# Performance work log

Hardware: AMD Instinct MI355X
Metric: run time of the kernel (lower is better)

## Reference

```python
import jax, jax.numpy as jnp
import numpy as np

B, S, DIM, HEADS, DHEAD = 1, 1992, 2048, 16, 128
NKI_SEQ_ALIGN = 128
EPS = 1e-6


def setup_inputs() -> dict:
    key = jax.random.key(0)
    ks = jax.random.split(key, 8)
    hidden_states = jax.random.normal(ks[0], (B, S, DIM), dtype=jnp.float32)
    # realistic rotary tables, full head_dim with interleaved pair angles
    pos = jnp.arange(S, dtype=jnp.float32)
    inv_freq = 1.0 / (10000.0 ** (jnp.arange(0, DHEAD, 2, dtype=jnp.float32) / DHEAD))
    ang = pos[:, None] * inv_freq[None, :]                      # [S, DHEAD/2]
    full = jnp.stack([ang, ang], axis=-1).reshape(S, DHEAD)     # interleave
    freqs_cos = jnp.cos(full)[None, :, None, :]                 # [1,S,1,DHEAD]
    freqs_sin = jnp.sin(full)[None, :, None, :]
    sc = 0.02
    wq = jax.random.normal(ks[1], (DIM, DIM), dtype=jnp.float32) * sc
    wk = jax.random.normal(ks[2], (DIM, DIM), dtype=jnp.float32) * sc
    wv = jax.random.normal(ks[3], (DIM, DIM), dtype=jnp.float32) * sc
    wo = jax.random.normal(ks[4], (DIM, DIM), dtype=jnp.float32) * sc
    bq = jax.random.normal(ks[5], (DIM,), dtype=jnp.float32) * sc
    bk = jax.random.normal(ks[6], (DIM,), dtype=jnp.float32) * sc
    bv = jax.random.normal(ks[7], (DIM,), dtype=jnp.float32) * sc
    bo = jnp.zeros((DIM,), dtype=jnp.float32)
    norm_q_w = jnp.ones((DIM,), dtype=jnp.float32)
    norm_k_w = jnp.ones((DIM,), dtype=jnp.float32)
    return dict(hidden_states=hidden_states, freqs_cos=freqs_cos, freqs_sin=freqs_sin,
                wq=wq, bq=bq, wk=wk, bk=bk, wv=wv, bv=bv,
                norm_q_w=norm_q_w, norm_k_w=norm_k_w, wo=wo, bo=bo)


def _rms_norm(x, weight, eps=EPS):
    xf = x.astype(jnp.float32)
    var = jnp.mean(xf * xf, axis=-1, keepdims=True)
    return (weight * (xf * jax.lax.rsqrt(var + eps))).astype(x.dtype)


def _apply_rope(x, freqs_cos, freqs_sin):
    # x: [B,H,S,D]; freqs: [1,S,1,D]
    cos = jnp.transpose(freqs_cos[..., 0::2], (0, 2, 1, 3))  # [1,1,S,D/2]
    sin = jnp.transpose(freqs_sin[..., 1::2], (0, 2, 1, 3))
    x1, x2 = x[..., 0::2], x[..., 1::2]
    o1 = x1 * cos - x2 * sin
    o2 = x1 * sin + x2 * cos
    return jnp.stack([o1, o2], axis=-1).reshape(x.shape)


def _attention_padded(q, k, v):
    # Faithful to nki_flash_attention: zero-pad seq to multiple of 128,
    # no masking of padded keys (they contribute logit 0), trim query pad.
    B_, H_, S_, D_ = q.shape
    pad = (-S_) % NKI_SEQ_ALIGN
    if pad:
        pc = [(0, 0), (0, 0), (0, pad), (0, 0)]
        q = jnp.pad(q, pc); k = jnp.pad(k, pc); v = jnp.pad(v, pc)
    scale = 1.0 / np.sqrt(D_)
    scores = jnp.einsum('bhqd,bhkd->bhqk', q, k) * scale
    probs = jax.nn.softmax(scores, axis=-1)
    out = jnp.einsum('bhqk,bhkd->bhqd', probs, v)
    return out[:, :, :S_, :]


def reference(hidden_states, freqs_cos, freqs_sin, wq, bq, wk, bk, wv, bv,
              norm_q_w, norm_k_w, wo, bo):
    b, s, _ = hidden_states.shape
    q = hidden_states @ wq.T + bq
    k = hidden_states @ wk.T + bk
    v = hidden_states @ wv.T + bv
    q = _rms_norm(q, norm_q_w)
    k = _rms_norm(k, norm_k_w)
    hd = q.shape[-1] // HEADS
    q = q.reshape(b, s, HEADS, hd).transpose(0, 2, 1, 3)
    k = k.reshape(b, s, HEADS, hd).transpose(0, 2, 1, 3)
    v = v.reshape(b, s, HEADS, hd).transpose(0, 2, 1, 3)
    q = _apply_rope(q, freqs_cos, freqs_sin)
    k = _apply_rope(k, freqs_cos, freqs_sin)
    o = _attention_padded(q, k, v)
    o = o.transpose(0, 2, 1, 3).reshape(b, s, -1)
    return o @ wo.T + bo
```

## Files before the change

kernel.cpp:

```cpp
#include <hip/hip_runtime.h>
#include <cstdint>

#define S_REAL 1992
#define S_PAD  2048
#define DIMSZ  2048
#define NHEAD  16
#define DHD    128

typedef float f32x4 __attribute__((ext_vector_type(4)));
typedef float f32x16 __attribute__((ext_vector_type(16)));
typedef __bf16 bf16x8 __attribute__((ext_vector_type(8)));
typedef unsigned short u16x8 __attribute__((ext_vector_type(8)));

__device__ __forceinline__ unsigned short f2bf(float f){
  uint32_t u = __float_as_uint(f);
  u += 0x7fffu + ((u >> 16) & 1u);
  return (unsigned short)(u >> 16);
}

__device__ __forceinline__ void gload16(const void* g, void* l){
  __builtin_amdgcn_global_load_lds(
      (const __attribute__((address_space(1))) uint32_t*)g,
      (__attribute__((address_space(3))) uint32_t*)l,
      16, 0, 0);
}

template<int N> __device__ __forceinline__ void waitbar(){
  if constexpr (N == 8)      asm volatile("s_waitcnt vmcnt(8)\n\ts_barrier" ::: "memory");
  else if constexpr (N == 6) asm volatile("s_waitcnt vmcnt(6)\n\ts_barrier" ::: "memory");
  else if constexpr (N == 4) asm volatile("s_waitcnt vmcnt(4)\n\ts_barrier" ::: "memory");
  else if constexpr (N == 3) asm volatile("s_waitcnt vmcnt(3)\n\ts_barrier" ::: "memory");
  else if constexpr (N == 2) asm volatile("s_waitcnt vmcnt(2)\n\ts_barrier" ::: "memory");
  else                       asm volatile("s_waitcnt vmcnt(0)\n\ts_barrier" ::: "memory");
}

__launch_bounds__(256)
__global__ void k_cvt5(const float* __restrict__ s0, const float* __restrict__ s1,
                       const float* __restrict__ s2, const float* __restrict__ s3,
                       const float* __restrict__ s4,
                       unsigned short* __restrict__ d0, unsigned short* __restrict__ d1,
                       unsigned short* __restrict__ d2, unsigned short* __restrict__ d3,
                       unsigned short* __restrict__ d4,
                       int nX, int nW)
{
  int i = blockIdx.x * 256 + threadIdx.x;
  const float* s; unsigned short* d; int j;
  if (i < nX){ s = s0; d = d0; j = i; }
  else {
    int k = i - nX;
    int wsel = k / nW; j = k - wsel * nW;
    s = (wsel == 0) ? s1 : (wsel == 1) ? s2 : (wsel == 2) ? s3 : s4;
    d = (wsel == 0) ? d1 : (wsel == 1) ? d2 : (wsel == 2) ? d3 : d4;
  }
  const float4* sp = (const float4*)s + (size_t)j * 2;
  float4 a = sp[0], b = sp[1];
  u16x8 o;
  o[0]=f2bf(a.x); o[1]=f2bf(a.y); o[2]=f2bf(a.z); o[3]=f2bf(a.w);
  o[4]=f2bf(b.x); o[5]=f2bf(b.y); o[6]=f2bf(b.z); o[7]=f2bf(b.w);
  *((u16x8*)d + j) = o;
}

__launch_bounds__(256, 3)
__global__ void k_g32(const unsigned short* __restrict__ A,
                      const unsigned short* __restrict__ B0,
                      const unsigned short* __restrict__ B1,
                      const unsigned short* __restrict__ B2,
                      const float* __restrict__ bias0,
                      const float* __restrict__ bias1,
                      const float* __restrict__ bias2,
                      float* __restrict__ C0, float* __restrict__ C1, float* __restrict__ C2,
                      int Mreal)
{
  constexpr int BUFE = 8192;
  constexpr int NT   = DIMSZ / 32;
  __shared__ unsigned short lds[3 * BUFE];

  const unsigned short* Bm = (blockIdx.z == 0) ? B0 : ((blockIdx.z == 1) ? B1 : B2);
  const float* bias        = (blockIdx.z == 0) ? bias0 : ((blockIdx.z == 1) ? bias1 : bias2);
  float* C                 = (blockIdx.z == 0) ? C0 : ((blockIdx.z == 1) ? C1 : C2);

  const int fid = blockIdx.x + gridDim.x * blockIdx.y;
  const int q   = (gridDim.x * gridDim.y) >> 3;
  const int nf  = (fid & 7) * q + (fid >> 3);
  const int m0  = (nf >> 4) * 128, n0 = (nf & 15) * 128;

  const int tid = threadIdx.x;
  const int w = tid >> 6, l = tid & 63;
  const int l31 = l & 31, l5 = l >> 5;
  const int wr = (w >> 1) * 64, wc = (w & 1) * 64;

  f32x16 acc[2][2];
  #pragma unroll
  for (int mb = 0; mb < 2; ++mb)
    #pragma unroll
    for (int nb = 0; nb < 2; ++nb)
      #pragma unroll
      for (int r = 0; r < 16; ++r) acc[mb][nb][r] = 0.f;

#define G32_STAGE(TT, BASE) do{                                                   \
    const int k0s = (TT) * 32;                                                    \
    unsigned short* dst = (BASE);                                                 \
    _Pragma("unroll")                                                             \
    for (int i_ = 0; i_ < 2; ++i_){                                               \
      int lin = i_ * 256 + tid;                                                   \
      int r_ = lin >> 2, pos_ = lin & 3;                                          \
      int gr_ = m0 + r_; if (gr_ > Mreal - 1) gr_ = Mreal - 1;                    \
      gload16(A + (size_t)gr_ * DIMSZ + k0s + (pos_ ^ ((r_ >> 1) & 3)) * 8,       \
              dst + lin * 8);                                                     \
    }                                                                             \
    _Pragma("unroll")                                                             \
    for (int i_ = 0; i_ < 2; ++i_){                                               \
      int lin = i_ * 256 + tid;                                                   \
      int r_ = lin >> 2, pos_ = lin & 3;                                          \
      gload16(Bm + (size_t)(n0 + r_) * DIMSZ + k0s + (pos_ ^ ((r_ >> 1) & 3)) * 8,\
              dst + 4096 + lin * 8);                                              \
    }                                                                             \
  } while(0)

#define G32_COMPUTE(BASE) do{                                                     \
    const unsigned short* sb = (BASE);                                            \
    bf16x8 a_[2][2], b_[2][2];                                                    \
    _Pragma("unroll")                                                             \
    for (int mb = 0; mb < 2; ++mb)                                                \
      _Pragma("unroll")                                                           \
      for (int ks = 0; ks < 2; ++ks){                                             \
        int r_ = wr + mb * 32 + l31;                                              \
        int c_ = (ks * 2 + l5) ^ ((r_ >> 1) & 3);                                 \
        a_[mb][ks] = *(const bf16x8*)(sb + r_ * 32 + c_ * 8);                     \
      }                                                                           \
    _Pragma("unroll")                                                             \
    for (int nb = 0; nb < 2; ++nb)                                                \
      _Pragma("unroll")                                                           \
      for (int ks = 0; ks < 2; ++ks){                                             \
        int r_ = wc + nb * 32 + l31;                                              \
        int c_ = (ks * 2 + l5) ^ ((r_ >> 1) & 3);                                 \
        b_[nb][ks] = *(const bf16x8*)(sb + 4096 + r_ * 32 + c_ * 8);              \
      }                                                                           \
    __builtin_amdgcn_s_setprio(1);                                                \
    _Pragma("unroll")                                                             \
    for (int ks = 0; ks < 2; ++ks)                                                \
      _Pragma("unroll")                                                           \
      for (int mb = 0; mb < 2; ++mb)                                              \
        _Pragma("unroll")                                                         \
        for (int nb = 0; nb < 2; ++nb)                                            \
          acc[mb][nb] = __builtin_amdgcn_mfma_f32_32x32x16_bf16(a_[mb][ks],       \
                            b_[nb][ks], acc[mb][nb], 0, 0, 0);                    \
    __builtin_amdgcn_s_setprio(0);                                                \
  } while(0)

  G32_STAGE(0, lds);
  G32_STAGE(1, lds + BUFE);
  int bc = 0, bs = 2;
  for (int tt = 0; tt < NT - 2; ++tt){
    waitbar<4>();
    G32_STAGE(tt + 2, lds + bs * BUFE);
    G32_COMPUTE(lds + bc * BUFE);
    bs = (bs == 2) ? 0 : bs + 1;
    bc = (bc == 2) ? 0 : bc + 1;
  }
  waitbar<4>();
  G32_COMPUTE(lds + bc * BUFE);
  bc = (bc == 2) ? 0 : bc + 1;
  waitbar<0>();
  G32_COMPUTE(lds + bc * BUFE);

#undef G32_STAGE
#undef G32_COMPUTE

  #pragma unroll
  for (int nb = 0; nb < 2; ++nb){
    int col = n0 + wc + nb * 32 + l31;
    float bz = bias[col];
    #pragma unroll
    for (int mb = 0; mb < 2; ++mb){
      #pragma unroll
      for (int r = 0; r < 16; ++r){
        int row = m0 + wr + mb * 32 + (r & 3) + 8 * (r >> 2) + 4 * l5;
        if (row < Mreal) C[(size_t)row * DIMSZ + col] = acc[mb][nb][r] + bz;
      }
    }
  }
}

__launch_bounds__(256)
__global__ void k_normrope2(const float* __restrict__ Qf, const float* __restrict__ Kf,
                            const float* __restrict__ nqw, const float* __restrict__ nkw,
                            const float* __restrict__ fc, const float* __restrict__ fs,
                            unsigned short* __restrict__ OutQ, unsigned short* __restrict__ OutK)
{
  const int s = blockIdx.x;
  const int isK = blockIdx.y;
  const float* Xf = isK ? Kf : Qf;
  const float* nw = isK ? nkw : nqw;
  unsigned short* Out = isK ? OutK : OutQ;
  const float scale = isK ? 1.0f : 0.08838834764831843f;
  const int swz = isK;

  const int t = threadIdx.x;
  const int w = t >> 6, l = t & 63;
  __shared__ float wred[4];
  float v[8];
  float ss = 0.f;
  if (s < S_REAL){
    const float4* p = (const float4*)(Xf + (size_t)s * DIMSZ) + t * 2;
    float4 a = p[0], b = p[1];
    v[0]=a.x; v[1]=a.y; v[2]=a.z; v[3]=a.w; v[4]=b.x; v[5]=b.y; v[6]=b.z; v[7]=b.w;
    #pragma unroll
    for (int j = 0; j < 8; ++j) ss += v[j] * v[j];
  }
  #pragma unroll
  for (int off = 32; off >= 1; off >>= 1) ss += __shfl_xor(ss, off);
  if (l == 0) wred[w] = ss;
  __syncthreads();
  float tot = wred[0] + wred[1] + wred[2] + wred[3];
  float rinv = rsqrtf(tot * (1.f / DIMSZ) + 1e-6f);

  const int h  = t >> 4;
  const int d0 = (t & 15) * 8;
  const int b  = t & 15;
  const int bsw = swz ? (b ^ (s & 7)) : b;
  unsigned short* dst = Out + ((size_t)h * S_PAD + s) * DHD + bsw * 8;
  u16x8 o;
  if (s < S_REAL){
    #pragma unroll
    for (int i = 0; i < 4; ++i){
      float c_ = fc[s * DHD + d0 + 2 * i];
      float s_ = fs[s * DHD + d0 + 2 * i + 1];
      float x1 = v[2 * i]     * rinv * nw[t * 8 + 2 * i];
      float x2 = v[2 * i + 1] * rinv * nw[t * 8 + 2 * i + 1];
      o[2 * i]     = f2bf((x1 * c_ - x2 * s_) * scale);
      o[2 * i + 1] = f2bf((x1 * s_ + x2 * c_) * scale);
    }
  } else {
    #pragma unroll
    for (int j = 0; j < 8; ++j) o[j] = 0;
  }
  *(u16x8*)dst = o;
}

__launch_bounds__(256)
__global__ void k_vtrans(const float* __restrict__ Vf, unsigned short* __restrict__ Vth)
{
  __shared__ unsigned short tile[64][72];
  const int t = threadIdx.x;
  const int s0 = blockIdx.x * 64, c0 = blockIdx.y * 64;
  #pragma unroll
  for (int i = 0; i < 4; ++i){
    int r = (t >> 4) * 4 + i;
    int s = s0 + r;
    int cq = (t & 15) * 4;
    float4 val = {0.f, 0.f, 0.f, 0.f};
    if (s < S_REAL) val = *((const float4*)(Vf + (size_t)s * DIMSZ + c0) + (t & 15));
    tile[r][cq + 0] = f2bf(val.x);
    tile[r][cq + 1] = f2bf(val.y);
    tile[r][cq + 2] = f2bf(val.z);
    tile[r][cq + 3] = f2bf(val.w);
  }
  __syncthreads();
  const int cl = t >> 2;
  const int cc = c0 + cl;
  #pragma unroll
  for (int bi = 0; bi < 2; ++bi){
    int b = (t & 3) * 2 + bi;
    u16x8 o;
    #pragma unroll
    for (int j = 0; j < 8; ++j) o[j] = tile[b * 8 + j][cl];
    int bsw = b ^ (cc & 7);
    *(u16x8*)(Vth + (size_t)cc * S_PAD + s0 + bsw * 8) = o;
  }
}

__launch_bounds__(256)
__global__ void k_attn(const unsigned short* __restrict__ Qh,
                       const unsigned short* __restrict__ Kh,
                       const unsigned short* __restrict__ Vth,
                       unsigned short* __restrict__ O)
{
  __shared__ unsigned short kbuf[2][64 * 128];
  __shared__ unsigned short vbuf[2][128 * 64];
  __shared__ unsigned short pbuf[4][16 * 64];
  const int h = blockIdx.y;
  const int q0 = blockIdx.x * 64;
  const int t = threadIdx.x, w = t >> 6, l = t & 63;
  const int lr = l & 15, lg = l >> 4;

  const unsigned short* Qp = Qh + ((size_t)h * S_PAD + q0 + w * 16 + lr) * DHD;
  bf16x8 qf[4];
  #pragma unroll
  for (int ks = 0; ks < 4; ++ks) qf[ks] = *(const bf16x8*)(Qp + ks * 32 + lg * 8);

  f32x4 acc[8];
  #pragma unroll
  for (int nf = 0; nf < 8; ++nf) acc[nf] = (f32x4){0.f, 0.f, 0.f, 0.f};
  float m = -3.0e38f, lsum = 0.f;

#define ATT_STAGE(KT, BI) do{                                                       \
    _Pragma("unroll")                                                               \
    for (int i_ = 0; i_ < 4; ++i_){                                                 \
      int rK = (w * 4 + i_) * 4 + (l >> 4);                                         \
      gload16(Kh + ((size_t)h * S_PAD + (KT) * 64 + rK) * DHD + (l & 15) * 8,       \
              &kbuf[BI][(w * 4 + i_) * 512]);                                       \
      int rV = (w * 4 + i_) * 8 + (l >> 3);                                         \
      gload16(Vth + ((size_t)h * DHD + rV) * S_PAD + (KT) * 64 + (l & 7) * 8,       \
              &vbuf[BI][(w * 4 + i_) * 512]);                                       \
    }                                                                               \
  } while(0)

  ATT_STAGE(0, 0);
  __syncthreads();

  for (int kt = 0; kt < S_PAD / 64; ++kt){
    const int bi = kt & 1;
    if (kt < S_PAD / 64 - 1) ATT_STAGE(kt + 1, bi ^ 1);

    f32x4 sf[4];
    __builtin_amdgcn_s_setprio(1);
    #pragma unroll
    for (int kvf = 0; kvf < 4; ++kvf){
      sf[kvf] = (f32x4){0.f, 0.f, 0.f, 0.f};
      int r = kvf * 16 + lr;
      #pragma unroll
      for (int ks = 0; ks < 4; ++ks){
        int blk = (ks * 4 + lg) ^ (r & 7);
        bf16x8 kf = *(const bf16x8*)&kbuf[bi][r * 128 + blk * 8];
        sf[kvf] = __builtin_amdgcn_mfma_f32_16x16x32_bf16(kf, qf[ks], sf[kvf], 0, 0, 0);
      }
    }
    __builtin_amdgcn_s_setprio(0);

    float pmax = sf[0][0];
    #pragma unroll
    for (int kvf = 0; kvf < 4; ++kvf)
      #pragma unroll
      for (int j = 0; j < 4; ++j) pmax = fmaxf(pmax, sf[kvf][j]);
    pmax = fmaxf(pmax, __shfl_xor(pmax, 16));
    pmax = fmaxf(pmax, __shfl_xor(pmax, 32));
    float mn = fmaxf(m, pmax);
    float fr = __expf(m - mn);
    m = mn;
    float p[4][4];
    float psum = 0.f;
    #pragma unroll
    for (int kvf = 0; kvf < 4; ++kvf)
      #pragma unroll
      for (int j = 0; j < 4; ++j){ p[kvf][j] = __expf(sf[kvf][j] - mn); psum += p[kvf][j]; }
    lsum = lsum * fr + psum;

    float fv0 = __shfl(fr, lg * 4 + 0);
    float fv1 = __shfl(fr, lg * 4 + 1);
    float fv2 = __shfl(fr, lg * 4 + 2);
    float fv3 = __shfl(fr, lg * 4 + 3);
    f32x4 fv = (f32x4){fv0, fv1, fv2, fv3};
    #pragma unroll
    for (int nf = 0; nf < 8; ++nf) acc[nf] *= fv;

    char* pb = (char*)pbuf[w];
    #pragma unroll
    for (int kvf = 0; kvf < 4; ++kvf){
      uint2 wv;
      wv.x = (uint32_t)f2bf(p[kvf][0]) | ((uint32_t)f2bf(p[kvf][1]) << 16);
      wv.y = (uint32_t)f2bf(p[kvf][2]) | ((uint32_t)f2bf(p[kvf][3]) << 16);
      int byte = lr * 128 + (((kvf * 2 + (lg >> 1)) ^ (lr & 7)) * 16) + (lg & 1) * 8;
      *(uint2*)(pb + byte) = wv;
    }
    bf16x8 pf[2];
    #pragma unroll
    for (int c = 0; c < 2; ++c)
      pf[c] = *(const bf16x8*)(pb + lr * 128 + ((c * 4 + lg) ^ (lr & 7)) * 16);

    __builtin_amdgcn_s_setprio(1);
    #pragma unroll
    for (int nf = 0; nf < 8; ++nf){
      int cc = nf * 16 + lr;
      #pragma unroll
      for (int ks = 0; ks < 2; ++ks){
        int blk = (ks * 4 + lg) ^ (cc & 7);
        bf16x8 vf = *(const bf16x8*)&vbuf[bi][cc * 64 + blk * 8];
        acc[nf] = __builtin_amdgcn_mfma_f32_16x16x32_bf16(pf[ks], vf, acc[nf], 0, 0, 0);
      }
    }
    __builtin_amdgcn_s_setprio(0);

    __syncthreads();
  }
#undef ATT_STAGE

  lsum += __shfl_xor(lsum, 16);
  lsum += __shfl_xor(lsum, 32);
  float ls0 = __shfl(lsum, lg * 4 + 0);
  float ls1 = __shfl(lsum, lg * 4 + 1);
  float ls2 = __shfl(lsum, lg * 4 + 2);
  float ls3 = __shfl(lsum, lg * 4 + 3);
  f32x4 lsv = (f32x4){1.f / ls0, 1.f / ls1, 1.f / ls2, 1.f / ls3};

  #pragma unroll
  for (int nf = 0; nf < 8; ++nf){
    #pragma unroll
    for (int j = 0; j < 4; ++j){
      int row = q0 + w * 16 + lg * 4 + j;
      if (row < S_REAL)
        O[(size_t)row * DIMSZ + h * DHD + nf * 16 + lr] = f2bf(acc[nf][j] * lsv[j]);
    }
  }
}

extern "C" void kernel_launch(void* const* d_in, const int* in_sizes, int n_in,
                              void* d_out, int out_size, void* d_ws, size_t ws_size,
                              hipStream_t stream)
{
  const float* hidden = (const float*)d_in[0];
  const float* fc  = (const float*)d_in[1];
  const float* fs  = (const float*)d_in[2];
  const float* wq  = (const float*)d_in[3];
  const float* bq  = (const float*)d_in[4];
  const float* wk  = (const float*)d_in[5];
  const float* bk  = (const float*)d_in[6];
  const float* wv  = (const float*)d_in[7];
  const float* bv  = (const float*)d_in[8];
  const float* nqw = (const float*)d_in[9];
  const float* nkw = (const float*)d_in[10];
  const float* wo  = (const float*)d_in[11];
  const float* bo  = (const float*)d_in[12];
  float* out = (float*)d_out;

  char* ws = (char*)d_ws;
  size_t off = 0;
  auto alloc = [&](size_t bytes) -> void* {
    void* p = ws + off;
    off += (bytes + 255) & ~(size_t)255;
    return p;
  };
  unsigned short* Xb  = (unsigned short*)alloc((size_t)S_REAL * DIMSZ * 2);
  unsigned short* Wqb = (unsigned short*)alloc((size_t)DIMSZ * DIMSZ * 2);
  unsigned short* Wkb = (unsigned short*)alloc((size_t)DIMSZ * DIMSZ * 2);
  unsigned short* Wvb = (unsigned short*)alloc((size_t)DIMSZ * DIMSZ * 2);
  unsigned short* Wob = (unsigned short*)alloc((size_t)DIMSZ * DIMSZ * 2);
  float* Qf = (float*)alloc((size_t)S_REAL * DIMSZ * 4);
  float* Kf = (float*)alloc((size_t)S_REAL * DIMSZ * 4);
  float* Vf = (float*)alloc((size_t)S_REAL * DIMSZ * 4);
  unsigned short* Qhh = (unsigned short*)alloc((size_t)NHEAD * S_PAD * DHD * 2);
  unsigned short* Khh = (unsigned short*)alloc((size_t)NHEAD * S_PAD * DHD * 2);
  unsigned short* Vth = (unsigned short*)alloc((size_t)NHEAD * DHD * S_PAD * 2);
  unsigned short* Oa  = (unsigned short*)alloc((size_t)S_REAL * DIMSZ * 2);

  {
    int nX = S_REAL * DIMSZ / 8;
    int nW = DIMSZ * DIMSZ / 8;
    int total = nX + 4 * nW;
    k_cvt5<<<total / 256, 256, 0, stream>>>(hidden, wq, wk, wv, wo,
                                            Xb, Wqb, Wkb, Wvb, Wob, nX, nW);
  }

  k_g32<<<dim3(16, 16, 3), 256, 0, stream>>>(Xb, Wqb, Wkb, Wvb, bq, bk, bv,
                                             Qf, Kf, Vf, S_REAL);

  k_normrope2<<<dim3(S_PAD, 2), 256, 0, stream>>>(Qf, Kf, nqw, nkw, fc, fs, Qhh, Khh);

  k_vtrans<<<dim3(S_PAD / 64, DIMSZ / 64), 256, 0, stream>>>(Vf, Vth);

  k_attn<<<dim3(S_PAD / 64, NHEAD), 256, 0, stream>>>(Qhh, Khh, Vth, Oa);

  k_g32<<<dim3(16, 16, 1), 256, 0, stream>>>(Oa, Wob, Wob, Wob, bo, bo, bo,
                                             out, out, out, S_REAL);
}
```

Baseline: 220.0 us.

## Emit V as bf16 from projection GEMM, widen attention blocks, lazy softmax rescale

The QKV GEMM now writes the V projection directly as bf16, so the transpose kernel reads half as many bytes and the fp32 V buffer is no longer needed. The attention kernel now runs 512 threads with 128 queries per block, which halves K/V tile reloads per query. Online-softmax rescaling of the accumulator is skipped when the running max grows by at most 8 across the wave. That skip changes how values are bounded, since exp(s-m) can reach e^8 in bf16 probabilities, and it adds a wave-wide vote in every tile.

```diff
diff --git a/kernel.cpp b/kernel.cpp
--- a/kernel.cpp
+++ b/kernel.cpp
@@ -26,12 +26,8 @@
 }
 
 template<int N> __device__ __forceinline__ void waitbar(){
-  if constexpr (N == 8)      asm volatile("s_waitcnt vmcnt(8)\n\ts_barrier" ::: "memory");
-  else if constexpr (N == 6) asm volatile("s_waitcnt vmcnt(6)\n\ts_barrier" ::: "memory");
-  else if constexpr (N == 4) asm volatile("s_waitcnt vmcnt(4)\n\ts_barrier" ::: "memory");
-  else if constexpr (N == 3) asm volatile("s_waitcnt vmcnt(3)\n\ts_barrier" ::: "memory");
-  else if constexpr (N == 2) asm volatile("s_waitcnt vmcnt(2)\n\ts_barrier" ::: "memory");
-  else                       asm volatile("s_waitcnt vmcnt(0)\n\ts_barrier" ::: "memory");
+  if constexpr (N == 4) asm volatile("s_waitcnt vmcnt(4)\n\ts_barrier" ::: "memory");
+  else                  asm volatile("s_waitcnt vmcnt(0)\n\ts_barrier" ::: "memory");
 }
 
 __launch_bounds__(256)
@@ -68,7 +64,8 @@
                       const float* __restrict__ bias0,
                       const float* __restrict__ bias1,
                       const float* __restrict__ bias2,
-                      float* __restrict__ C0, float* __restrict__ C1, float* __restrict__ C2,
+                      float* __restrict__ C0, float* __restrict__ C1,
+                      unsigned short* __restrict__ Cb,
                       int Mreal)
 {
   constexpr int BUFE = 8192;
@@ -77,7 +74,7 @@
 
   const unsigned short* Bm = (blockIdx.z == 0) ? B0 : ((blockIdx.z == 1) ? B1 : B2);
   const float* bias        = (blockIdx.z == 0) ? bias0 : ((blockIdx.z == 1) ? bias1 : bias2);
-  float* C                 = (blockIdx.z == 0) ? C0 : ((blockIdx.z == 1) ? C1 : C2);
+  float* C                 = (blockIdx.z == 0) ? C0 : C1;
 
   const int fid = blockIdx.x + gridDim.x * blockIdx.y;
   const int q   = (gridDim.x * gridDim.y) >> 3;
@@ -167,6 +164,7 @@
 #undef G32_STAGE
 #undef G32_COMPUTE
 
+  const bool vout = (blockIdx.z == 2);
   #pragma unroll
   for (int nb = 0; nb < 2; ++nb){
     int col = n0 + wc + nb * 32 + l31;
@@ -176,7 +174,10 @@
       #pragma unroll
       for (int r = 0; r < 16; ++r){
         int row = m0 + wr + mb * 32 + (r & 3) + 8 * (r >> 2) + 4 * l5;
-        if (row < Mreal) C[(size_t)row * DIMSZ + col] = acc[mb][nb][r] + bz;
+        if (row < Mreal){
+          if (vout) Cb[(size_t)row * DIMSZ + col] = f2bf(acc[mb][nb][r] + bz);
+          else      C[(size_t)row * DIMSZ + col] = acc[mb][nb][r] + bz;
+        }
       }
     }
   }
@@ -239,22 +240,19 @@
 }
 
 __launch_bounds__(256)
-__global__ void k_vtrans(const float* __restrict__ Vf, unsigned short* __restrict__ Vth)
+__global__ void k_vtrans(const unsigned short* __restrict__ Vb, unsigned short* __restrict__ Vth)
 {
   __shared__ unsigned short tile[64][72];
   const int t = threadIdx.x;
   const int s0 = blockIdx.x * 64, c0 = blockIdx.y * 64;
   #pragma unroll
-  for (int i = 0; i < 4; ++i){
-    int r = (t >> 4) * 4 + i;
-    int s = s0 + r;
-    int cq = (t & 15) * 4;
-    float4 val = {0.f, 0.f, 0.f, 0.f};
-    if (s < S_REAL) val = *((const float4*)(Vf + (size_t)s * DIMSZ + c0) + (t & 15));
-    tile[r][cq + 0] = f2bf(val.x);
-    tile[r][cq + 1] = f2bf(val.y);
-    tile[r][cq + 2] = f2bf(val.z);
-    tile[r][cq + 3] = f2bf(val.w);
+  for (int i = 0; i < 2; ++i){
+    int lin = i * 256 + t;
+    int r = lin >> 3, ck = lin & 7;
+    u16x8 val = (u16x8){0,0,0,0,0,0,0,0};
+    if (s0 + r < S_REAL)
+      val = *(const u16x8*)(Vb + (size_t)(s0 + r) * DIMSZ + c0 + ck * 8);
+    *(u16x8*)&tile[r][ck * 8] = val;
   }
   __syncthreads();
   const int cl = t >> 2;
@@ -270,7 +268,7 @@
   }
 }
 
-__launch_bounds__(256)
+__launch_bounds__(512)
 __global__ void k_attn(const unsigned short* __restrict__ Qh,
                        const unsigned short* __restrict__ Kh,
                        const unsigned short* __restrict__ Vth,
@@ -278,9 +276,9 @@
 {
   __shared__ unsigned short kbuf[2][64 * 128];
   __shared__ unsigned short vbuf[2][128 * 64];
-  __shared__ unsigned short pbuf[4][16 * 64];
+  __shared__ unsigned short pbuf[8][16 * 64];
   const int h = blockIdx.y;
-  const int q0 = blockIdx.x * 64;
+  const int q0 = blockIdx.x * 128;
   const int t = threadIdx.x, w = t >> 6, l = t & 63;
   const int lr = l & 15, lg = l >> 4;
 
@@ -296,13 +294,18 @@
 
 #define ATT_STAGE(KT, BI) do{                                                       \
     _Pragma("unroll")                                                               \
-    for (int i_ = 0; i_ < 4; ++i_){                                                 \
-      int rK = (w * 4 + i_) * 4 + (l >> 4);                                         \
-      gload16(Kh + ((size_t)h * S_PAD + (KT) * 64 + rK) * DHD + (l & 15) * 8,       \
-              &kbuf[BI][(w * 4 + i_) * 512]);                                       \
-      int rV = (w * 4 + i_) * 8 + (l >> 3);                                         \
-      gload16(Vth + ((size_t)h * DHD + rV) * S_PAD + (KT) * 64 + (l & 7) * 8,       \
-              &vbuf[BI][(w * 4 + i_) * 512]);                                       \
+    for (int i_ = 0; i_ < 2; ++i_){                                                 \
+      int lin = i_ * 512 + t;                                                       \
+      int rK = lin >> 4, ckK = lin & 15;                                            \
+      gload16(Kh + ((size_t)h * S_PAD + (KT) * 64 + rK) * DHD + ckK * 8,            \
+              &kbuf[BI][lin * 8]);                                                  \
+    }                                                                               \
+    _Pragma("unroll")                                                               \
+    for (int i_ = 0; i_ < 2; ++i_){                                                 \
+      int lin = i_ * 512 + t;                                                       \
+      int rV = lin >> 3, ckV = lin & 7;                                             \
+      gload16(Vth + ((size_t)h * DHD + rV) * S_PAD + (KT) * 64 + ckV * 8,           \
+              &vbuf[BI][lin * 8]);                                                  \
     }                                                                               \
   } while(0)
 
@@ -335,24 +338,28 @@
       for (int j = 0; j < 4; ++j) pmax = fmaxf(pmax, sf[kvf][j]);
     pmax = fmaxf(pmax, __shfl_xor(pmax, 16));
     pmax = fmaxf(pmax, __shfl_xor(pmax, 32));
-    float mn = fmaxf(m, pmax);
-    float fr = __expf(m - mn);
-    m = mn;
+
+    float fr = 1.f;
+    if (!__all(pmax - m <= 8.0f)){
+      float mn = fmaxf(m, pmax);
+      fr = __expf(m - mn);
+      m = mn;
+      float fv0 = __shfl(fr, lg * 4 + 0);
+      float fv1 = __shfl(fr, lg * 4 + 1);
+      float fv2 = __shfl(fr, lg * 4 + 2);
+      float fv3 = __shfl(fr, lg * 4 + 3);
+      f32x4 fv = (f32x4){fv0, fv1, fv2, fv3};
+      #pragma unroll
+      for (int nf = 0; nf < 8; ++nf) acc[nf] *= fv;
+    }
+
     float p[4][4];
     float psum = 0.f;
     #pragma unroll
     for (int kvf = 0; kvf < 4; ++kvf)
       #pragma unroll
-      for (int j = 0; j < 4; ++j){ p[kvf][j] = __expf(sf[kvf][j] - mn); psum += p[kvf][j]; }
+      for (int j = 0; j < 4; ++j){ p[kvf][j] = __expf(sf[kvf][j] - m); psum += p[kvf][j]; }
     lsum = lsum * fr + psum;
-
-    float fv0 = __shfl(fr, lg * 4 + 0);
-    float fv1 = __shfl(fr, lg * 4 + 1);
-    float fv2 = __shfl(fr, lg * 4 + 2);
-    float fv3 = __shfl(fr, lg * 4 + 3);
-    f32x4 fv = (f32x4){fv0, fv1, fv2, fv3};
-    #pragma unroll
-    for (int nf = 0; nf < 8; ++nf) acc[nf] *= fv;
 
     char* pb = (char*)pbuf[w];
     #pragma unroll
@@ -437,7 +444,7 @@
   unsigned short* Wob = (unsigned short*)alloc((size_t)DIMSZ * DIMSZ * 2);
   float* Qf = (float*)alloc((size_t)S_REAL * DIMSZ * 4);
   float* Kf = (float*)alloc((size_t)S_REAL * DIMSZ * 4);
-  float* Vf = (float*)alloc((size_t)S_REAL * DIMSZ * 4);
+  unsigned short* Vb  = (unsigned short*)alloc((size_t)S_REAL * DIMSZ * 2);
   unsigned short* Qhh = (unsigned short*)alloc((size_t)NHEAD * S_PAD * DHD * 2);
   unsigned short* Khh = (unsigned short*)alloc((size_t)NHEAD * S_PAD * DHD * 2);
   unsigned short* Vth = (unsigned short*)alloc((size_t)NHEAD * DHD * S_PAD * 2);
@@ -452,14 +459,14 @@
   }
 
   k_g32<<<dim3(16, 16, 3), 256, 0, stream>>>(Xb, Wqb, Wkb, Wvb, bq, bk, bv,
-                                             Qf, Kf, Vf, S_REAL);
+                                             Qf, Kf, Vb, S_REAL);
 
   k_normrope2<<<dim3(S_PAD, 2), 256, 0, stream>>>(Qf, Kf, nqw, nkw, fc, fs, Qhh, Khh);
 
-  k_vtrans<<<dim3(S_PAD / 64, DIMSZ / 64), 256, 0, stream>>>(Vf, Vth);
-
-  k_attn<<<dim3(S_PAD / 64, NHEAD), 256, 0, stream>>>(Qhh, Khh, Vth, Oa);
+  k_vtrans<<<dim3(S_PAD / 64, DIMSZ / 64), 256, 0, stream>>>(Vb, Vth);
+
+  k_attn<<<dim3(S_PAD / 128, NHEAD), 512, 0, stream>>>(Qhh, Khh, Vth, Oa);
 
   k_g32<<<dim3(16, 16, 1), 256, 0, stream>>>(Oa, Wob, Wob, Wob, bo, bo, bo,
-                                             out, out, out, S_REAL);
-}
+                                             out, out, nullptr, S_REAL);
+}
```

New measurement: 220.7 us. No clear change (+0.3%).
